# Optimization experiments

Measured on AMD Instinct MI355X. Metric: run time of the kernel, lower is better.

Reference implementation:

```python
import jax, jax.numpy as jnp
import numpy as np

INPUT_SIZE, HIDDEN, OUT = 2, 32, 1

def setup_inputs() -> dict:
    key = jax.random.key(0)
    ks = jax.random.split(key, 8)
    B, T = 2048, 512
    s_ih = 1.0 / np.sqrt(HIDDEN)
    return {
        "x": jax.random.normal(ks[0], (B, T, INPUT_SIZE), dtype=jnp.float32),
        "W_ih": jax.random.uniform(ks[1], (4 * HIDDEN, INPUT_SIZE), minval=-s_ih, maxval=s_ih, dtype=jnp.float32),
        "W_hh": jax.random.uniform(ks[2], (4 * HIDDEN, HIDDEN), minval=-s_ih, maxval=s_ih, dtype=jnp.float32),
        "b_ih": jax.random.uniform(ks[3], (4 * HIDDEN,), minval=-s_ih, maxval=s_ih, dtype=jnp.float32),
        "b_hh": jax.random.uniform(ks[4], (4 * HIDDEN,), minval=-s_ih, maxval=s_ih, dtype=jnp.float32),
        "W_fc": jax.random.uniform(ks[5], (OUT, HIDDEN), minval=-s_ih, maxval=s_ih, dtype=jnp.float32),
        "b_fc": jax.random.uniform(ks[6], (OUT,), minval=-s_ih, maxval=s_ih, dtype=jnp.float32),
    }

def _lstm(x, W_ih, W_hh, b_ih, b_hh):
    # x: [B, T, I]; PyTorch gate order: i, f, g, o
    B, T, _ = x.shape
    H = W_hh.shape[1]
    # precompute input projections for all timesteps: [T, B, 4H]
    xp = jnp.einsum('bti,gi->tbg', x, W_ih) + (b_ih + b_hh)

    def step(carry, xp_t):
        h, c = carry
        gates = xp_t + h @ W_hh.T  # [B, 4H]
        i, f, g, o = jnp.split(gates, 4, axis=-1)
        i = jax.nn.sigmoid(i)
        f = jax.nn.sigmoid(f)
        g = jnp.tanh(g)
        o = jax.nn.sigmoid(o)
        c = f * c + i * g
        h = o * jnp.tanh(c)
        return (h, c), h

    h0 = jnp.zeros((B, H), dtype=x.dtype)
    c0 = jnp.zeros((B, H), dtype=x.dtype)
    _, hs = jax.lax.scan(step, (h0, c0), xp)  # hs: [T, B, H]
    return jnp.transpose(hs, (1, 0, 2))  # [B, T, H]

def reference(x, W_ih, W_hh, b_ih, b_hh, W_fc, b_fc):
    lstm_out = _lstm(x, W_ih, W_hh, b_ih, b_hh)  # [B, T, H]
    return lstm_out @ W_fc.T + b_fc  # [B, T, OUT]
```

## Files before the change

### kernel.cpp

```cpp
#include <hip/hip_runtime.h>


#define BB 2048
#define TT 512
#define HH 32
#define CHUNK 32
#define ROWF 36
#define EPAD 4
#define WSTRIDE (2 * CHUNK * ROWF + EPAD)

#define LOG2E 1.44269504088896340736f

typedef float v2f __attribute__((ext_vector_type(2)));
typedef float v4f __attribute__((ext_vector_type(4)));

__device__ __forceinline__ float sigm2(float xs) {
    return __builtin_amdgcn_rcpf(1.0f + __builtin_amdgcn_exp2f(-xs));
}

__global__ __launch_bounds__(256, 1) void lstm_fused_kernel(
    const float* __restrict__ x,
    const float* __restrict__ W_ih,
    const float* __restrict__ W_hh,
    const float* __restrict__ b_ih,
    const float* __restrict__ b_hh,
    const float* __restrict__ W_fc,
    const float* __restrict__ b_fc,
    float* __restrict__ out)
{
    __shared__ __align__(16) float lds_h[4][WSTRIDE];

    const int lane = threadIdx.x & 63;
    const int wv   = threadIdx.x >> 6;
    const int elem = lane >> 5;
    const int j    = lane & 31;
    const int b    = blockIdx.x * 8 + wv * 2 + elem;

    const int ri = j, rf = HH + j, rg = 2 * HH + j, ro = 3 * HH + j;
    const float si = LOG2E;
    const float sg = 2.0f * LOG2E;

    const v2f wihI = ((const v2f*)W_ih)[ri] * si;
    const v2f wihF = ((const v2f*)W_ih)[rf] * si;
    const v2f wihG = ((const v2f*)W_ih)[rg] * sg;
    const v2f wihO = ((const v2f*)W_ih)[ro] * si;
    const float bI = (b_ih[ri] + b_hh[ri]) * si;
    const float bF = (b_ih[rf] + b_hh[rf]) * si;
    const float bG = (b_ih[rg] + b_hh[rg]) * sg;
    const float bO = (b_ih[ro] + b_hh[ro]) * si;

    v2f wI[HH / 2], wF[HH / 2], wG[HH / 2], wO[HH / 2];
    #pragma unroll
    for (int k = 0; k < HH / 2; ++k) {
        wI[k] = ((const v2f*)(W_hh + ri * HH))[k] * si;
        wF[k] = ((const v2f*)(W_hh + rf * HH))[k] * si;
        wG[k] = ((const v2f*)(W_hh + rg * HH))[k] * sg;
        wO[k] = ((const v2f*)(W_hh + ro * HH))[k] * si;
    }

    float wfc[HH];
    #pragma unroll
    for (int u = 0; u < HH; ++u) wfc[u] = W_fc[u];
    const float bfc = b_fc[0];

    float c = 0.0f;

    float* hb = &lds_h[wv][elem * (CHUNK * ROWF + EPAD)];
    float* wr = hb + j;
    const float* rd = hb + (CHUNK - 1) * ROWF;

    wr[(CHUNK - 1) * ROWF] = 0.0f;

    const float* xb = x + (size_t)b * (TT * 2);
    float* outp = out + (size_t)b * TT + j;

    v4f xq0 = *(const v4f*)(xb);
    v4f xq1 = *(const v4f*)(xb + 4);

    const v2f bI2 = {bI, 0.0f}, bF2 = {bF, 0.0f};
    const v2f bG2 = {bG, 0.0f}, bO2 = {bO, 0.0f};

    #pragma unroll 1
    for (int ch = 0; ch < TT / CHUNK; ++ch) {
        #pragma unroll 1
        for (int uu = 0; uu < CHUNK; uu += 4) {
            const int t = ch * CHUNK + uu;
            const float* xnx = (t + 4 < TT) ? (xb + (t + 4) * 2) : xb;
            v4f nxq0 = *(const v4f*)(xnx);
            v4f nxq1 = *(const v4f*)(xnx + 4);

            #pragma unroll
            for (int s = 0; s < 4; ++s) {
                v4f hq[8];
                const v4f* rq = (const v4f*)rd;
                #pragma unroll
                for (int q = 0; q < 8; ++q) hq[q] = rq[q];

                v2f xt;
                if      (s == 0) xt = (v2f){xq0.x, xq0.y};
                else if (s == 1) xt = (v2f){xq0.z, xq0.w};
                else if (s == 2) xt = (v2f){xq1.x, xq1.y};
                else             xt = (v2f){xq1.z, xq1.w};

                v2f aI0 = __builtin_elementwise_fma(xt, wihI, bI2);
                v2f aF0 = __builtin_elementwise_fma(xt, wihF, bF2);
                v2f aG0 = __builtin_elementwise_fma(xt, wihG, bG2);
                v2f aO0 = __builtin_elementwise_fma(xt, wihO, bO2);
                v2f aI1, aF1, aG1, aO1;

                #pragma unroll
                for (int k = 0; k < HH / 2; ++k) {
                    v2f hp = (k & 1)
                        ? __builtin_shufflevector(hq[k >> 1], hq[k >> 1], 2, 3)
                        : __builtin_shufflevector(hq[k >> 1], hq[k >> 1], 0, 1);
                    if (k < HH / 4) {
                        aI0 = __builtin_elementwise_fma(hp, wI[k], aI0);
                        aF0 = __builtin_elementwise_fma(hp, wF[k], aF0);
                        aG0 = __builtin_elementwise_fma(hp, wG[k], aG0);
                        aO0 = __builtin_elementwise_fma(hp, wO[k], aO0);
                    } else if (k == HH / 4) {
                        aI1 = hp * wI[k]; aF1 = hp * wF[k];
                        aG1 = hp * wG[k]; aO1 = hp * wO[k];
                    } else {
                        aI1 = __builtin_elementwise_fma(hp, wI[k], aI1);
                        aF1 = __builtin_elementwise_fma(hp, wF[k], aF1);
                        aG1 = __builtin_elementwise_fma(hp, wG[k], aG1);
                        aO1 = __builtin_elementwise_fma(hp, wO[k], aO1);
                    }
                }
                v2f aI = aI0 + aI1, aF = aF0 + aF1;
                v2f aG = aG0 + aG1, aO = aO0 + aO1;
                float gi = aI.x + aI.y;
                float gf = aF.x + aF.y;
                float gg = aG.x + aG.y;
                float go = aO.x + aO.y;

                float iv = sigm2(gi);
                float fv = sigm2(gf);
                float ov = sigm2(go);
                float gv = fmaf(4.0f * LOG2E, sigm2(gg), -2.0f * LOG2E);

                c = fmaf(fv, c, iv * gv);

                float rr   = sigm2(c);
                float ov2  = ov + ov;
                float hnew = fmaf(ov2, rr, -ov);

                *wr = hnew;
                rd = wr - j;
                wr += ROWF;
            }
            xq0 = nxq0; xq1 = nxq1;
        }

        wr -= CHUNK * ROWF;

        float acc = bfc;
        const float* row = hb + j * ROWF;
        #pragma unroll
        for (int u = 0; u < HH; ++u)
            acc = fmaf(row[u], wfc[u], acc);
        *outp = acc;
        outp += CHUNK;
    }
}

extern "C" void kernel_launch(void* const* d_in, const int* in_sizes, int n_in,
                              void* d_out, int out_size, void* d_ws, size_t ws_size,
                              hipStream_t stream) {
    const float* x    = (const float*)d_in[0];
    const float* W_ih = (const float*)d_in[1];
    const float* W_hh = (const float*)d_in[2];
    const float* b_ih = (const float*)d_in[3];
    const float* b_hh = (const float*)d_in[4];
    const float* W_fc = (const float*)d_in[5];
    const float* b_fc = (const float*)d_in[6];
    float* out = (float*)d_out;

    dim3 grid(BB / 8);
    dim3 block(256);
    lstm_fused_kernel<<<grid, block, 0, stream>>>(x, W_ih, W_hh, b_ih, b_hh,
                                                  W_fc, b_fc, out);
}
```

Measured before the change: 205.5 us.

## Store hidden state in fp16 LDS and use packed fdot2 for recurrence

Converts W_hh and W_fc to half precision in registers, stores h in LDS as fp16, and computes the gate matvec and output projection with v_dot2 (fdot2) instructions that accumulate in fp32. This halves the LDS read traffic per step and halves the number of multiply-accumulate instructions on the sequential critical path. The h reload is moved right after the store so it can overlap with the next step's input projection. It adds fp16 rounding error on h and the weights, which compounds across 512 timesteps and may break the accuracy tolerance.

Result: faster. 194.1 us (-5.5%).

```diff
diff --git a/kernel.cpp b/kernel.cpp
--- a/kernel.cpp
+++ b/kernel.cpp
@@ -5,18 +5,33 @@
 #define TT 512
 #define HH 32
 #define CHUNK 32
-#define ROWF 36
-#define EPAD 4
-#define WSTRIDE (2 * CHUNK * ROWF + EPAD)
+#define ROWH 40
+#define WSH (2 * CHUNK * ROWH + 8)
 
 #define LOG2E 1.44269504088896340736f
 
 typedef float v2f __attribute__((ext_vector_type(2)));
 typedef float v4f __attribute__((ext_vector_type(4)));
+typedef unsigned int v4u __attribute__((ext_vector_type(4)));
+typedef _Float16 h2 __attribute__((ext_vector_type(2)));
 
 __device__ __forceinline__ float sigm2(float xs) {
     return __builtin_amdgcn_rcpf(1.0f + __builtin_amdgcn_exp2f(-xs));
 }
+
+__device__ __forceinline__ h2 u2h(unsigned int u) {
+    return __builtin_bit_cast(h2, u);
+}
+
+#if defined(__has_builtin)
+#if __has_builtin(__builtin_amdgcn_fdot2)
+#define FDOT2(a, b, c) __builtin_amdgcn_fdot2((a), (b), (c), false)
+#endif
+#endif
+#ifndef FDOT2
+#define FDOT2(a, b, c) fmaf((float)(a).y, (float)(b).y, \
+                            fmaf((float)(a).x, (float)(b).x, (c)))
+#endif
 
 __global__ __launch_bounds__(256, 1) void lstm_fused_kernel(
     const float* __restrict__ x,
@@ -28,13 +43,13 @@
     const float* __restrict__ b_fc,
     float* __restrict__ out)
 {
-    __shared__ __align__(16) float lds_h[4][WSTRIDE];
+    __shared__ __align__(16) _Float16 lds_h[4][WSH];
 
     const int lane = threadIdx.x & 63;
     const int wv   = threadIdx.x >> 6;
-    const int elem = lane >> 5;
     const int j    = lane & 31;
-    const int b    = blockIdx.x * 8 + wv * 2 + elem;
+    const bool low = (lane < 32);
+    const int b    = blockIdx.x * 8 + wv * 2 + (low ? 0 : 1);
 
     const int ri = j, rf = HH + j, rg = 2 * HH + j, ro = 3 * HH + j;
     const float si = LOG2E;
@@ -49,36 +64,47 @@
     const float bG = (b_ih[rg] + b_hh[rg]) * sg;
     const float bO = (b_ih[ro] + b_hh[ro]) * si;
 
-    v2f wI[HH / 2], wF[HH / 2], wG[HH / 2], wO[HH / 2];
+    h2 wI[16], wF[16], wG[16], wO[16];
     #pragma unroll
-    for (int k = 0; k < HH / 2; ++k) {
-        wI[k] = ((const v2f*)(W_hh + ri * HH))[k] * si;
-        wF[k] = ((const v2f*)(W_hh + rf * HH))[k] * si;
-        wG[k] = ((const v2f*)(W_hh + rg * HH))[k] * sg;
-        wO[k] = ((const v2f*)(W_hh + ro * HH))[k] * si;
-    }
-
-    float wfc[HH];
+    for (int k = 0; k < 16; ++k) {
+        v2f a;
+        a = ((const v2f*)(W_hh + ri * HH))[k] * si;
+        wI[k] = (h2){(_Float16)a.x, (_Float16)a.y};
+        a = ((const v2f*)(W_hh + rf * HH))[k] * si;
+        wF[k] = (h2){(_Float16)a.x, (_Float16)a.y};
+        a = ((const v2f*)(W_hh + rg * HH))[k] * sg;
+        wG[k] = (h2){(_Float16)a.x, (_Float16)a.y};
+        a = ((const v2f*)(W_hh + ro * HH))[k] * si;
+        wO[k] = (h2){(_Float16)a.x, (_Float16)a.y};
+    }
+
+    h2 wfc2[16];
     #pragma unroll
-    for (int u = 0; u < HH; ++u) wfc[u] = W_fc[u];
+    for (int k = 0; k < 16; ++k) {
+        v2f a = ((const v2f*)W_fc)[k];
+        wfc2[k] = (h2){(_Float16)a.x, (_Float16)a.y};
+    }
     const float bfc = b_fc[0];
 
     float c = 0.0f;
 
-    float* hb = &lds_h[wv][elem * (CHUNK * ROWF + EPAD)];
-    float* wr = hb + j;
-    const float* rd = hb + (CHUNK - 1) * ROWF;
-
-    wr[(CHUNK - 1) * ROWF] = 0.0f;
+    _Float16* hb = &lds_h[wv][low ? 0 : CHUNK * ROWH];
+    _Float16* wr = hb + j;
+
+    hb[(CHUNK - 1) * ROWH + j] = (_Float16)0.0f;
+
+    v4u hq[4];
+    {
+        const v4u* rq = (const v4u*)(hb + (CHUNK - 1) * ROWH);
+        #pragma unroll
+        for (int q = 0; q < 4; ++q) hq[q] = rq[q];
+    }
 
     const float* xb = x + (size_t)b * (TT * 2);
     float* outp = out + (size_t)b * TT + j;
 
     v4f xq0 = *(const v4f*)(xb);
     v4f xq1 = *(const v4f*)(xb + 4);
-
-    const v2f bI2 = {bI, 0.0f}, bF2 = {bF, 0.0f};
-    const v2f bG2 = {bG, 0.0f}, bO2 = {bO, 0.0f};
 
     #pragma unroll 1
     for (int ch = 0; ch < TT / CHUNK; ++ch) {
@@ -91,49 +117,42 @@
 
             #pragma unroll
             for (int s = 0; s < 4; ++s) {
-                v4f hq[8];
-                const v4f* rq = (const v4f*)rd;
-                #pragma unroll
-                for (int q = 0; q < 8; ++q) hq[q] = rq[q];
-
                 v2f xt;
                 if      (s == 0) xt = (v2f){xq0.x, xq0.y};
                 else if (s == 1) xt = (v2f){xq0.z, xq0.w};
                 else if (s == 2) xt = (v2f){xq1.x, xq1.y};
                 else             xt = (v2f){xq1.z, xq1.w};
 
-                v2f aI0 = __builtin_elementwise_fma(xt, wihI, bI2);
-                v2f aF0 = __builtin_elementwise_fma(xt, wihF, bF2);
-                v2f aG0 = __builtin_elementwise_fma(xt, wihG, bG2);
-                v2f aO0 = __builtin_elementwise_fma(xt, wihO, bO2);
-                v2f aI1, aF1, aG1, aO1;
+                float aI0 = fmaf(xt.y, wihI.y, fmaf(xt.x, wihI.x, bI));
+                float aF0 = fmaf(xt.y, wihF.y, fmaf(xt.x, wihF.x, bF));
+                float aG0 = fmaf(xt.y, wihG.y, fmaf(xt.x, wihG.x, bG));
+                float aO0 = fmaf(xt.y, wihO.y, fmaf(xt.x, wihO.x, bO));
+                float aI1, aF1, aG1, aO1;
 
                 #pragma unroll
-                for (int k = 0; k < HH / 2; ++k) {
-                    v2f hp = (k & 1)
-                        ? __builtin_shufflevector(hq[k >> 1], hq[k >> 1], 2, 3)
-                        : __builtin_shufflevector(hq[k >> 1], hq[k >> 1], 0, 1);
-                    if (k < HH / 4) {
-                        aI0 = __builtin_elementwise_fma(hp, wI[k], aI0);
-                        aF0 = __builtin_elementwise_fma(hp, wF[k], aF0);
-                        aG0 = __builtin_elementwise_fma(hp, wG[k], aG0);
-                        aO0 = __builtin_elementwise_fma(hp, wO[k], aO0);
-                    } else if (k == HH / 4) {
-                        aI1 = hp * wI[k]; aF1 = hp * wF[k];
-                        aG1 = hp * wG[k]; aO1 = hp * wO[k];
+                for (int k = 0; k < 16; ++k) {
+                    h2 hp = u2h(hq[k >> 2][k & 3]);
+                    if (k < 8) {
+                        aI0 = FDOT2(hp, wI[k], aI0);
+                        aF0 = FDOT2(hp, wF[k], aF0);
+                        aG0 = FDOT2(hp, wG[k], aG0);
+                        aO0 = FDOT2(hp, wO[k], aO0);
+                    } else if (k == 8) {
+                        aI1 = FDOT2(hp, wI[k], 0.0f);
+                        aF1 = FDOT2(hp, wF[k], 0.0f);
+                        aG1 = FDOT2(hp, wG[k], 0.0f);
+                        aO1 = FDOT2(hp, wO[k], 0.0f);
                     } else {
-                        aI1 = __builtin_elementwise_fma(hp, wI[k], aI1);
-                        aF1 = __builtin_elementwise_fma(hp, wF[k], aF1);
-                        aG1 = __builtin_elementwise_fma(hp, wG[k], aG1);
-                        aO1 = __builtin_elementwise_fma(hp, wO[k], aO1);
+                        aI1 = FDOT2(hp, wI[k], aI1);
+                        aF1 = FDOT2(hp, wF[k], aF1);
+                        aG1 = FDOT2(hp, wG[k], aG1);
+                        aO1 = FDOT2(hp, wO[k], aO1);
                     }
                 }
-                v2f aI = aI0 + aI1, aF = aF0 + aF1;
-                v2f aG = aG0 + aG1, aO = aO0 + aO1;
-                float gi = aI.x + aI.y;
-                float gf = aF.x + aF.y;
-                float gg = aG.x + aG.y;
-                float go = aO.x + aO.y;
+                float gi = aI0 + aI1;
+                float gf = aF0 + aF1;
+                float gg = aG0 + aG1;
+                float go = aO0 + aO1;
 
                 float iv = sigm2(gi);
                 float fv = sigm2(gf);
@@ -143,25 +162,33 @@
                 c = fmaf(fv, c, iv * gv);
 
                 float rr   = sigm2(c);
-                float ov2  = ov + ov;
-                float hnew = fmaf(ov2, rr, -ov);
-
-                *wr = hnew;
-                rd = wr - j;
-                wr += ROWF;
+                float hnew = fmaf(ov + ov, rr, -ov);
+
+                *wr = (_Float16)hnew;
+                {
+                    const v4u* rq = (const v4u*)(wr - j);
+                    #pragma unroll
+                    for (int q = 0; q < 4; ++q) hq[q] = rq[q];
+                }
+                wr += ROWH;
             }
             xq0 = nxq0; xq1 = nxq1;
         }
 
-        wr -= CHUNK * ROWF;
-
-        float acc = bfc;
-        const float* row = hb + j * ROWF;
-        #pragma unroll
-        for (int u = 0; u < HH; ++u)
-            acc = fmaf(row[u], wfc[u], acc);
-        *outp = acc;
-        outp += CHUNK;
+        wr -= CHUNK * ROWH;
+
+        {
+            const v4u* fr = (const v4u*)(hb + j * ROWH);
+            v4u f[4];
+            #pragma unroll
+            for (int q = 0; q < 4; ++q) f[q] = fr[q];
+            float acc = bfc;
+            #pragma unroll
+            for (int k = 0; k < 16; ++k)
+                acc = FDOT2(u2h(f[k >> 2][k & 3]), wfc2[k], acc);
+            *outp = acc;
+            outp += CHUNK;
+        }
     }
 }
 
```
